# Kernel optimization log

Hardware: AMD Instinct MI355X
Metric: run time of the kernel (lower is better)

## Reference

```python
import jax, jax.numpy as jnp
import numpy as np

NEG_INF = -1e9  # fp32-safe mask value for non-edges
ALPHA = 0.2     # LeakyReLU negative slope


def setup_inputs() -> dict:
    key = jax.random.key(0)
    k1, k2, k3, k4, k5 = jax.random.split(key, 5)
    N, F_in, H, F_out = 4096, 512, 8, 64
    features = jax.random.normal(k1, (N, F_in), dtype=jnp.float32)
    adjacency_matrix = jax.random.randint(k2, (N, N), 0, 2, dtype=jnp.int32)
    W = jax.random.normal(k3, (H, F_in, F_out), dtype=jnp.float32) * (F_in ** -0.5)
    a_src = jax.random.normal(k4, (H, F_out), dtype=jnp.float32) * (F_out ** -0.5)
    a_dst = jax.random.normal(k5, (H, F_out), dtype=jnp.float32) * (F_out ** -0.5)
    return {"features": features, "adjacency_matrix": adjacency_matrix,
            "W": W, "a_src": a_src, "a_dst": a_dst}


def reference(features, adjacency_matrix, W, a_src, a_dst):
    # Per-head linear projection: [H, N, F_out]
    Wh = jnp.einsum('nf,hfo->hno', features, W)
    # Attention logits e_ij = LeakyReLU(a_src . Wh_i + a_dst . Wh_j)
    src = jnp.einsum('hno,ho->hn', Wh, a_src)  # [H, N]
    dst = jnp.einsum('hno,ho->hn', Wh, a_dst)  # [H, N]
    e = jax.nn.leaky_relu(src[:, :, None] + dst[:, None, :], ALPHA)  # [H, N, N]
    mask = (adjacency_matrix > 0)[None, :, :]
    e = jnp.where(mask, e, jnp.asarray(NEG_INF, e.dtype))
    attn = jax.nn.softmax(e, axis=-1)  # adjacency-masked row softmax
    h = jnp.einsum('hij,hjo->hio', attn, Wh)  # [H, N, F_out]
    h = jax.nn.elu(h)
    # concat=True: torch.cat over feature dim -> [N, H*F_out]
    return jnp.transpose(h, (1, 0, 2)).reshape(h.shape[1], -1)
```

## Files before the change

kernel.cpp:

```cpp
#include <hip/hip_runtime.h>
#include <hip/hip_bf16.h>

typedef __bf16 bf16x8 __attribute__((ext_vector_type(8)));
typedef float  f32x4  __attribute__((ext_vector_type(4)));
typedef unsigned short u16x8 __attribute__((ext_vector_type(8)));
typedef unsigned short us4   __attribute__((ext_vector_type(4)));

#define HH    8
#define NN    4096
#define FIN   512
#define FOUT  64
#define ALPHA 0.2f

__global__ __launch_bounds__(256) void k_pack(int* __restrict__ adj) {
    const size_t base = (size_t)blockIdx.x * 8192;
    const int    tid  = threadIdx.x;
    unsigned m = 0;
#pragma unroll
    for (int p = 0; p < 8; ++p) {
        int4 v = *(const int4*)(adj + base + tid * 32 + p * 4);
        m |= (unsigned)(v.x > 0) << (p * 4);
        m |= (unsigned)(v.y > 0) << (p * 4 + 1);
        m |= (unsigned)(v.z > 0) << (p * 4 + 2);
        m |= (unsigned)(v.w > 0) << (p * 4 + 3);
    }
    __syncthreads();
    ((unsigned*)adj)[base + tid] = m;
}

__global__ __launch_bounds__(256) void k_transpose_w(
    const float* __restrict__ Wsrc, __hip_bfloat16* __restrict__ WT) {
    __shared__ __hip_bfloat16 lt[64][65];
    const int h  = blockIdx.x >> 3;
    const int f0 = (blockIdx.x & 7) * 64;
    const int tid = threadIdx.x;
#pragma unroll
    for (int p = 0; p < 16; ++p) {
        int f = p * 4 + (tid >> 6);
        int o = tid & 63;
        lt[f][o] = __float2bfloat16(Wsrc[((size_t)h * FIN + f0 + f) * FOUT + o]);
    }
    __syncthreads();
#pragma unroll
    for (int p = 0; p < 16; ++p) {
        int o = p * 4 + (tid >> 6);
        int f = tid & 63;
        WT[((size_t)h * FOUT + o) * FIN + f0 + f] = lt[f][o];
    }
}

__global__ __launch_bounds__(256) void k_proj(
    const float* __restrict__ feat,
    const __hip_bfloat16* __restrict__ WT,
    const float* __restrict__ a_src,
    const float* __restrict__ a_dst,
    unsigned short* __restrict__ WhT,
    float* __restrict__ srcv,
    unsigned short* __restrict__ Ebf, unsigned short* __restrict__ Fbf) {
    __shared__ alignas(16) __hip_bfloat16 lfeat[32][520];

    const int tid  = threadIdx.x;
    const int tile = blockIdx.x;

#pragma unroll
    for (int p = 0; p < 16; ++p) {
        int idx  = p * 256 + tid;
        int row  = idx >> 7;
        int col4 = (idx & 127) * 4;
        float4 f = *(const float4*)(feat + (size_t)(tile * 32 + row) * FIN + col4);
        __hip_bfloat16* dst = &lfeat[row][col4];
        dst[0] = __float2bfloat16(f.x); dst[1] = __float2bfloat16(f.y);
        dst[2] = __float2bfloat16(f.z); dst[3] = __float2bfloat16(f.w);
    }
    __syncthreads();

    const int h     = blockIdx.y * 4 + (tid >> 6);
    const int lane  = tid & 63;
    const int row16 = lane & 15;
    const int quad  = lane >> 4;

    const unsigned short* WTu = (const unsigned short*)WT + (size_t)h * FOUT * FIN;

    f32x4 acc[2][4] = {};
    for (int k0 = 0; k0 < FIN; k0 += 32) {
        bf16x8 a0 = *(const bf16x8*)&lfeat[row16][k0 + quad * 8];
        bf16x8 a1 = *(const bf16x8*)&lfeat[16 + row16][k0 + quad * 8];
#pragma unroll
        for (int ot = 0; ot < 4; ++ot) {
            bf16x8 b = *(const bf16x8*)(WTu + (size_t)(ot * 16 + row16) * FIN + k0 + quad * 8);
            acc[0][ot] = __builtin_amdgcn_mfma_f32_16x16x32_bf16(a0, b, acc[0][ot], 0, 0, 0);
            acc[1][ot] = __builtin_amdgcn_mfma_f32_16x16x32_bf16(a1, b, acc[1][ot], 0, 0, 0);
        }
    }

#pragma unroll
    for (int g = 0; g < 2; ++g)
#pragma unroll
        for (int ot = 0; ot < 4; ++ot) {
            us4 u;
#pragma unroll
            for (int r = 0; r < 4; ++r)
                u[r] = __builtin_bit_cast(unsigned short, (__bf16)acc[g][ot][r]);
            *(us4*)(WhT + (size_t)(h * FOUT + ot * 16 + row16) * NN
                        + tile * 32 + g * 16 + quad * 4) = u;
        }

    float asv[4], adv[4];
#pragma unroll
    for (int ot = 0; ot < 4; ++ot) {
        asv[ot] = a_src[h * FOUT + ot * 16 + row16];
        adv[ot] = a_dst[h * FOUT + ot * 16 + row16];
    }
#pragma unroll
    for (int g = 0; g < 2; ++g)
#pragma unroll
        for (int r = 0; r < 4; ++r) {
            float ss = 0.f, dd = 0.f;
#pragma unroll
            for (int ot = 0; ot < 4; ++ot) {
                ss += acc[g][ot][r] * asv[ot];
                dd += acc[g][ot][r] * adv[ot];
            }
            ss += __shfl_xor(ss, 1); ss += __shfl_xor(ss, 2);
            ss += __shfl_xor(ss, 4); ss += __shfl_xor(ss, 8);
            dd += __shfl_xor(dd, 1); dd += __shfl_xor(dd, 2);
            dd += __shfl_xor(dd, 4); dd += __shfl_xor(dd, 8);
            if (row16 == 0) {
                int n = tile * 32 + g * 16 + quad * 4 + r;
                srcv[h * NN + n] = ss;
                __bf16 e = (__bf16)__expf(dd);
                __bf16 f = (__bf16)__expf(ALPHA * dd);
                Ebf[h * NN + n] = __builtin_bit_cast(unsigned short, e);
                Fbf[h * NN + n] = __builtin_bit_cast(unsigned short, f);
            }
        }
}

__global__ __launch_bounds__(512, 2) void k_flash(
    const unsigned* __restrict__ maskp,
    const float* __restrict__ srcv,
    const unsigned short* __restrict__ Ebf,
    const unsigned short* __restrict__ Fbf,
    const unsigned short* __restrict__ WhT,
    float* __restrict__ out) {
    __shared__ float lds_stash[2][2][4096];
    __shared__ float lds_l[2][2][64];

    unsigned* lmask = (unsigned*)&lds_stash[0][0][0];

    const int tid   = threadIdx.x;
    const int wv    = tid >> 6;
    const int lane  = tid & 63;
    const int row16 = lane & 15;
    const int quad  = lane >> 4;
    const int h2    = wv & 1;
    const int seg   = wv >> 1;

    const int bx   = blockIdx.x;
    const int hg   = (bx >> 3) & 3;
    const int tile = ((bx >> 5) << 3) | (bx & 7);

#pragma unroll
    for (int p = 0; p < 4; ++p) {
        int tt = tid + p * 512;
        int c  = tt >> 6;
        int o  = (tt & 63) * 16;
        int4 v = *(const int4*)((const char*)maskp
                                + (size_t)(tile * 32 + c) * 32768 + o);
        int row = c * 2 + (o >> 9);
        int dw  = (o & 511) >> 2;
        *(int4*)&lmask[row * 132 + dw] = v;
    }
    __syncthreads();

    const int h   = hg * 2 + h2;
    const int shl = quad * 8;

    float Es[4], Fs[4];
    const unsigned* lm[4];
#pragma unroll
    for (int g = 0; g < 4; ++g) {
        float si = srcv[h * NN + tile * 64 + g * 16 + row16];
        Es[g] = __expf(si);
        Fs[g] = __expf(ALPHA * si);
        lm[g] = &lmask[(g * 16 + row16) * 132 + seg * 32];
    }

    const unsigned short* Eb = Ebf + h * NN + seg * 1024;
    const unsigned short* Fb = Fbf + h * NN + seg * 1024;
    const unsigned short* wh = WhT + (size_t)h * FOUT * NN + seg * 1024;

    bf16x8 ones;
#pragma unroll
    for (int k = 0; k < 8; ++k) ones[k] = (__bf16)1.0f;

    f32x4 acc[4][4] = {};
    f32x4 accl[4]   = {};

#pragma unroll 1
    for (int t = 0; t < 32; ++t) {
        int jj = t * 32 + shl;
        u16x8 ev = *(const u16x8*)(Eb + jj);
        u16x8 fv = *(const u16x8*)(Fb + jj);
        unsigned mb[4];
#pragma unroll
        for (int g = 0; g < 4; ++g) mb[g] = (lm[g][t] >> shl) & 0xffu;

        bf16x8 af[4];
#pragma unroll
        for (int k = 0; k < 8; ++k) {
            float ef = __uint_as_float((unsigned)ev[k] << 16);
            float ff = __uint_as_float((unsigned)fv[k] << 16);
#pragma unroll
            for (int g = 0; g < 4; ++g) {
                float p = fmaxf(ef * Es[g], ff * Fs[g]);
                af[g][k] = (__bf16)(((mb[g] >> k) & 1u) ? p : 0.f);
            }
        }
        bf16x8 b[4];
#pragma unroll
        for (int ot = 0; ot < 4; ++ot)
            b[ot] = *(const bf16x8*)(wh + (size_t)(ot * 16 + row16) * NN + jj);
#pragma unroll
        for (int g = 0; g < 4; ++g) {
#pragma unroll
            for (int ot = 0; ot < 4; ++ot)
                acc[g][ot] = __builtin_amdgcn_mfma_f32_16x16x32_bf16(af[g], b[ot], acc[g][ot], 0, 0, 0);
            accl[g] = __builtin_amdgcn_mfma_f32_16x16x32_bf16(af[g], ones, accl[g], 0, 0, 0);
        }
    }

    __syncthreads();

    if (seg == 1 || seg == 3) {
        float* st = &lds_stash[seg >> 1][h2][0];
#pragma unroll
        for (int g = 0; g < 4; ++g)
#pragma unroll
            for (int ot = 0; ot < 4; ++ot)
#pragma unroll
                for (int r = 0; r < 4; ++r)
                    st[(g * 16 + quad * 4 + r) * 64 + ot * 16 + row16] = acc[g][ot][r];
        if (row16 == 0)
#pragma unroll
            for (int g = 0; g < 4; ++g)
#pragma unroll
                for (int r = 0; r < 4; ++r)
                    lds_l[seg >> 1][h2][g * 16 + quad * 4 + r] = accl[g][r];
    }
    __syncthreads();
    if (seg == 0 || seg == 2) {
        const float* st = &lds_stash[seg >> 1][h2][0];
#pragma unroll
        for (int g = 0; g < 4; ++g) {
#pragma unroll
            for (int ot = 0; ot < 4; ++ot)
#pragma unroll
                for (int r = 0; r < 4; ++r)
                    acc[g][ot][r] += st[(g * 16 + quad * 4 + r) * 64 + ot * 16 + row16];
#pragma unroll
            for (int r = 0; r < 4; ++r)
                accl[g][r] += lds_l[seg >> 1][h2][g * 16 + quad * 4 + r];
        }
    }
    __syncthreads();
    if (seg == 2) {
        float* st = &lds_stash[0][h2][0];
#pragma unroll
        for (int g = 0; g < 4; ++g)
#pragma unroll
            for (int ot = 0; ot < 4; ++ot)
#pragma unroll
                for (int r = 0; r < 4; ++r)
                    st[(g * 16 + quad * 4 + r) * 64 + ot * 16 + row16] = acc[g][ot][r];
        if (row16 == 0)
#pragma unroll
            for (int g = 0; g < 4; ++g)
#pragma unroll
                for (int r = 0; r < 4; ++r)
                    lds_l[0][h2][g * 16 + quad * 4 + r] = accl[g][r];
    }
    __syncthreads();
    if (seg == 0) {
        const float* st = &lds_stash[0][h2][0];
#pragma unroll
        for (int g = 0; g < 4; ++g)
#pragma unroll
            for (int r = 0; r < 4; ++r) {
                int   gqr = g * 16 + quad * 4 + r;
                float l   = accl[g][r] + lds_l[0][h2][gqr];
                float rl  = 1.0f / l;
#pragma unroll
                for (int ot = 0; ot < 4; ++ot) {
                    int   c = ot * 16 + row16;
                    float v = (acc[g][ot][r] + st[gqr * 64 + c]) * rl;
                    float y = v > 0.f ? v : __expf(v) - 1.f;
                    out[(size_t)(tile * 64 + gqr) * (HH * FOUT) + h * FOUT + c] = y;
                }
            }
    }
}

extern "C" void kernel_launch(void* const* d_in, const int* in_sizes, int n_in,
                              void* d_out, int out_size, void* d_ws, size_t ws_size,
                              hipStream_t stream) {
    const float* features = (const float*)d_in[0];
    int*         adj      = (int*)d_in[1];
    const float* W        = (const float*)d_in[2];
    const float* a_src    = (const float*)d_in[3];
    const float* a_dst    = (const float*)d_in[4];
    float*       out      = (float*)d_out;

    char* ws = (char*)d_ws;
    __hip_bfloat16* WT   = (__hip_bfloat16*)(ws);
    unsigned short* WhT  = (unsigned short*)(ws + (512 << 10));
    float*          srcv = (float*)(ws + (512 << 10) + (4 << 20));
    unsigned short* Ebf  = (unsigned short*)(ws + (512 << 10) + (4 << 20) + (128 << 10));
    unsigned short* Fbf  = (unsigned short*)(ws + (512 << 10) + (4 << 20) + (192 << 10));

    k_pack<<<dim3((NN * NN) / 8192), 256, 0, stream>>>(adj);
    k_transpose_w<<<dim3(64), 256, 0, stream>>>(W, WT);
    k_proj<<<dim3(NN / 32, 2), 256, 0, stream>>>(features, WT, a_src, a_dst,
                                                 WhT, srcv, Ebf, Fbf);
    k_flash<<<dim3(256), 512, 0, stream>>>((const unsigned*)adj, srcv, Ebf, Fbf,
                                           WhT, out);
}
```

Measured before the change: 176.0 us.

## Fuse mask packing into projection launch and retile flash kernel per head

```diff
diff --git a/kernel.cpp b/kernel.cpp
--- a/kernel.cpp
+++ b/kernel.cpp
@@ -11,22 +11,6 @@
 #define FIN   512
 #define FOUT  64
 #define ALPHA 0.2f
-
-__global__ __launch_bounds__(256) void k_pack(int* __restrict__ adj) {
-    const size_t base = (size_t)blockIdx.x * 8192;
-    const int    tid  = threadIdx.x;
-    unsigned m = 0;
-#pragma unroll
-    for (int p = 0; p < 8; ++p) {
-        int4 v = *(const int4*)(adj + base + tid * 32 + p * 4);
-        m |= (unsigned)(v.x > 0) << (p * 4);
-        m |= (unsigned)(v.y > 0) << (p * 4 + 1);
-        m |= (unsigned)(v.z > 0) << (p * 4 + 2);
-        m |= (unsigned)(v.w > 0) << (p * 4 + 3);
-    }
-    __syncthreads();
-    ((unsigned*)adj)[base + tid] = m;
-}
 
 __global__ __launch_bounds__(256) void k_transpose_w(
     const float* __restrict__ Wsrc, __hip_bfloat16* __restrict__ WT) {
@@ -49,7 +33,8 @@
     }
 }
 
-__global__ __launch_bounds__(256) void k_proj(
+__global__ __launch_bounds__(256) void k_prep(
+    int* __restrict__ adj,
     const float* __restrict__ feat,
     const __hip_bfloat16* __restrict__ WT,
     const float* __restrict__ a_src,
@@ -59,8 +44,27 @@
     unsigned short* __restrict__ Ebf, unsigned short* __restrict__ Fbf) {
     __shared__ alignas(16) __hip_bfloat16 lfeat[32][520];
 
-    const int tid  = threadIdx.x;
-    const int tile = blockIdx.x;
+    const int tid = threadIdx.x;
+
+    if (blockIdx.x < 2048) {
+        const size_t base = (size_t)blockIdx.x * 8192;
+        unsigned m = 0;
+#pragma unroll
+        for (int p = 0; p < 8; ++p) {
+            int4 v = *(const int4*)(adj + base + tid * 32 + p * 4);
+            m |= (unsigned)(v.x > 0) << (p * 4);
+            m |= (unsigned)(v.y > 0) << (p * 4 + 1);
+            m |= (unsigned)(v.z > 0) << (p * 4 + 2);
+            m |= (unsigned)(v.w > 0) << (p * 4 + 3);
+        }
+        __syncthreads();
+        ((unsigned*)adj)[base + tid] = m;
+        return;
+    }
+
+    const int pb   = blockIdx.x - 2048;
+    const int tile = pb & 127;
+    const int hgy  = pb >> 7;
 
 #pragma unroll
     for (int p = 0; p < 16; ++p) {
@@ -74,7 +78,7 @@
     }
     __syncthreads();
 
-    const int h     = blockIdx.y * 4 + (tid >> 6);
+    const int h     = hgy * 4 + (tid >> 6);
     const int lane  = tid & 63;
     const int row16 = lane & 15;
     const int quad  = lane >> 4;
@@ -143,161 +147,168 @@
     const unsigned short* __restrict__ Fbf,
     const unsigned short* __restrict__ WhT,
     float* __restrict__ out) {
-    __shared__ float lds_stash[2][2][4096];
-    __shared__ float lds_l[2][2][64];
-
-    unsigned* lmask = (unsigned*)&lds_stash[0][0][0];
+    __shared__ float st[2][128 * 68];
+    __shared__ float lds_l[2][128];
+
+    unsigned* lmask = (unsigned*)&st[0][0];
 
     const int tid   = threadIdx.x;
-    const int wv    = tid >> 6;
+    const int seg   = tid >> 6;
     const int lane  = tid & 63;
     const int row16 = lane & 15;
     const int quad  = lane >> 4;
-    const int h2    = wv & 1;
-    const int seg   = wv >> 1;
-
-    const int bx   = blockIdx.x;
-    const int hg   = (bx >> 3) & 3;
-    const int tile = ((bx >> 5) << 3) | (bx & 7);
-
-#pragma unroll
-    for (int p = 0; p < 4; ++p) {
+    const int shl   = quad * 8;
+    const int tile  = blockIdx.x;
+    const int h     = blockIdx.y;
+
+#pragma unroll
+    for (int p = 0; p < 8; ++p) {
         int tt = tid + p * 512;
         int c  = tt >> 6;
         int o  = (tt & 63) * 16;
         int4 v = *(const int4*)((const char*)maskp
-                                + (size_t)(tile * 32 + c) * 32768 + o);
+                                + (size_t)(tile * 64 + c) * 32768 + o);
         int row = c * 2 + (o >> 9);
         int dw  = (o & 511) >> 2;
         *(int4*)&lmask[row * 132 + dw] = v;
     }
     __syncthreads();
 
-    const int h   = hg * 2 + h2;
-    const int shl = quad * 8;
-
-    float Es[4], Fs[4];
-    const unsigned* lm[4];
-#pragma unroll
-    for (int g = 0; g < 4; ++g) {
-        float si = srcv[h * NN + tile * 64 + g * 16 + row16];
+    float Es[8], Fs[8];
+#pragma unroll
+    for (int g = 0; g < 8; ++g) {
+        float si = srcv[h * NN + tile * 128 + g * 16 + row16];
         Es[g] = __expf(si);
         Fs[g] = __expf(ALPHA * si);
-        lm[g] = &lmask[(g * 16 + row16) * 132 + seg * 32];
-    }
-
-    const unsigned short* Eb = Ebf + h * NN + seg * 1024;
-    const unsigned short* Fb = Fbf + h * NN + seg * 1024;
-    const unsigned short* wh = WhT + (size_t)h * FOUT * NN + seg * 1024;
+    }
+    const int mbase = row16 * 132 + seg * 16;
+
+    const unsigned short* Eb = Ebf + h * NN + seg * 512;
+    const unsigned short* Fb = Fbf + h * NN + seg * 512;
+    const unsigned short* wh = WhT + (size_t)h * FOUT * NN + seg * 512;
 
     bf16x8 ones;
 #pragma unroll
     for (int k = 0; k < 8; ++k) ones[k] = (__bf16)1.0f;
 
-    f32x4 acc[4][4] = {};
-    f32x4 accl[4]   = {};
+    f32x4 acc[8][4] = {};
+    f32x4 accl[8]   = {};
 
 #pragma unroll 1
-    for (int t = 0; t < 32; ++t) {
+    for (int t = 0; t < 16; ++t) {
         int jj = t * 32 + shl;
         u16x8 ev = *(const u16x8*)(Eb + jj);
         u16x8 fv = *(const u16x8*)(Fb + jj);
-        unsigned mb[4];
-#pragma unroll
-        for (int g = 0; g < 4; ++g) mb[g] = (lm[g][t] >> shl) & 0xffu;
-
-        bf16x8 af[4];
-#pragma unroll
-        for (int k = 0; k < 8; ++k) {
-            float ef = __uint_as_float((unsigned)ev[k] << 16);
-            float ff = __uint_as_float((unsigned)fv[k] << 16);
-#pragma unroll
-            for (int g = 0; g < 4; ++g) {
-                float p = fmaxf(ef * Es[g], ff * Fs[g]);
-                af[g][k] = (__bf16)(((mb[g] >> k) & 1u) ? p : 0.f);
-            }
-        }
         bf16x8 b[4];
 #pragma unroll
         for (int ot = 0; ot < 4; ++ot)
             b[ot] = *(const bf16x8*)(wh + (size_t)(ot * 16 + row16) * NN + jj);
-#pragma unroll
-        for (int g = 0; g < 4; ++g) {
+
+        float ef[8], ff[8];
+#pragma unroll
+        for (int k = 0; k < 8; ++k) {
+            ef[k] = __uint_as_float((unsigned)ev[k] << 16);
+            ff[k] = __uint_as_float((unsigned)fv[k] << 16);
+        }
+
+#pragma unroll
+        for (int gp = 0; gp < 4; ++gp) {
+            const int g0 = gp * 2, g1 = g0 + 1;
+            unsigned mb0 = (lmask[mbase + g0 * 2112 + t] >> shl) & 0xffu;
+            unsigned mb1 = (lmask[mbase + g1 * 2112 + t] >> shl) & 0xffu;
+            bf16x8 af0, af1;
+#pragma unroll
+            for (int k = 0; k < 8; ++k) {
+                float p0 = fmaxf(ef[k] * Es[g0], ff[k] * Fs[g0]);
+                float p1 = fmaxf(ef[k] * Es[g1], ff[k] * Fs[g1]);
+                af0[k] = (__bf16)(((mb0 >> k) & 1u) ? p0 : 0.f);
+                af1[k] = (__bf16)(((mb1 >> k) & 1u) ? p1 : 0.f);
+            }
+#pragma unroll
+            for (int ot = 0; ot < 4; ++ot) {
+                acc[g0][ot] = __builtin_amdgcn_mfma_f32_16x16x32_bf16(af0, b[ot], acc[g0][ot], 0, 0, 0);
+                acc[g1][ot] = __builtin_amdgcn_mfma_f32_16x16x32_bf16(af1, b[ot], acc[g1][ot], 0, 0, 0);
+            }
+            accl[g0] = __builtin_amdgcn_mfma_f32_16x16x32_bf16(af0, ones, accl[g0], 0, 0, 0);
+            accl[g1] = __builtin_amdgcn_mfma_f32_16x16x32_bf16(af1, ones, accl[g1], 0, 0, 0);
+        }
+    }
+
+    __syncthreads();
+
+    auto stash = [&](int buf) {
+#pragma unroll
+        for (int g = 0; g < 8; ++g)
 #pragma unroll
             for (int ot = 0; ot < 4; ++ot)
-                acc[g][ot] = __builtin_amdgcn_mfma_f32_16x16x32_bf16(af[g], b[ot], acc[g][ot], 0, 0, 0);
-            accl[g] = __builtin_amdgcn_mfma_f32_16x16x32_bf16(af[g], ones, accl[g], 0, 0, 0);
-        }
-    }
-
-    __syncthreads();
-
-    if (seg == 1 || seg == 3) {
-        float* st = &lds_stash[seg >> 1][h2][0];
-#pragma unroll
-        for (int g = 0; g < 4; ++g)
+#pragma unroll
+                for (int r = 0; r < 4; ++r)
+                    st[buf][(g * 16 + quad * 4 + r) * 68 + ot * 16 + row16] = acc[g][ot][r];
+        if (row16 == 0)
+#pragma unroll
+            for (int g = 0; g < 8; ++g)
+#pragma unroll
+                for (int r = 0; r < 4; ++r)
+                    lds_l[buf][g * 16 + quad * 4 + r] = accl[g][r];
+    };
+    auto addin = [&](int buf) {
+#pragma unroll
+        for (int g = 0; g < 8; ++g) {
 #pragma unroll
             for (int ot = 0; ot < 4; ++ot)
 #pragma unroll
                 for (int r = 0; r < 4; ++r)
-                    st[(g * 16 + quad * 4 + r) * 64 + ot * 16 + row16] = acc[g][ot][r];
-        if (row16 == 0)
-#pragma unroll
-            for (int g = 0; g < 4; ++g)
-#pragma unroll
-                for (int r = 0; r < 4; ++r)
-                    lds_l[seg >> 1][h2][g * 16 + quad * 4 + r] = accl[g][r];
-    }
-    __syncthreads();
-    if (seg == 0 || seg == 2) {
-        const float* st = &lds_stash[seg >> 1][h2][0];
-#pragma unroll
-        for (int g = 0; g < 4; ++g) {
-#pragma unroll
-            for (int ot = 0; ot < 4; ++ot)
-#pragma unroll
-                for (int r = 0; r < 4; ++r)
-                    acc[g][ot][r] += st[(g * 16 + quad * 4 + r) * 64 + ot * 16 + row16];
+                    acc[g][ot][r] += st[buf][(g * 16 + quad * 4 + r) * 68 + ot * 16 + row16];
 #pragma unroll
             for (int r = 0; r < 4; ++r)
-                accl[g][r] += lds_l[seg >> 1][h2][g * 16 + quad * 4 + r];
-        }
-    }
-    __syncthreads();
-    if (seg == 2) {
-        float* st = &lds_stash[0][h2][0];
-#pragma unroll
-        for (int g = 0; g < 4; ++g)
-#pragma unroll
-            for (int ot = 0; ot < 4; ++ot)
-#pragma unroll
-                for (int r = 0; r < 4; ++r)
-                    st[(g * 16 + quad * 4 + r) * 64 + ot * 16 + row16] = acc[g][ot][r];
-        if (row16 == 0)
-#pragma unroll
-            for (int g = 0; g < 4; ++g)
-#pragma unroll
-                for (int r = 0; r < 4; ++r)
-                    lds_l[0][h2][g * 16 + quad * 4 + r] = accl[g][r];
-    }
+                accl[g][r] += lds_l[buf][g * 16 + quad * 4 + r];
+        }
+    };
+
+    if (seg == 1) stash(0);
+    if (seg == 3) stash(1);
+    __syncthreads();
+    if (seg == 0) addin(0);
+    if (seg == 2) addin(1);
+    __syncthreads();
+    if (seg == 5) stash(0);
+    if (seg == 7) stash(1);
+    __syncthreads();
+    if (seg == 4) addin(0);
+    if (seg == 6) addin(1);
+    __syncthreads();
+    if (seg == 2) stash(0);
+    if (seg == 6) stash(1);
+    __syncthreads();
+    if (seg == 0) addin(0);
+    if (seg == 4) addin(1);
+    __syncthreads();
+    if (seg == 4) stash(0);
     __syncthreads();
     if (seg == 0) {
-        const float* st = &lds_stash[0][h2][0];
-#pragma unroll
-        for (int g = 0; g < 4; ++g)
+        addin(0);
+#pragma unroll
+        for (int g = 0; g < 8; ++g)
 #pragma unroll
             for (int r = 0; r < 4; ++r) {
                 int   gqr = g * 16 + quad * 4 + r;
-                float l   = accl[g][r] + lds_l[0][h2][gqr];
-                float rl  = 1.0f / l;
+                float rl  = 1.0f / accl[g][r];
 #pragma unroll
                 for (int ot = 0; ot < 4; ++ot) {
-                    int   c = ot * 16 + row16;
-                    float v = (acc[g][ot][r] + st[gqr * 64 + c]) * rl;
+                    float v = acc[g][ot][r] * rl;
                     float y = v > 0.f ? v : __expf(v) - 1.f;
-                    out[(size_t)(tile * 64 + gqr) * (HH * FOUT) + h * FOUT + c] = y;
+                    st[0][gqr * 68 + ot * 16 + row16] = y;
                 }
             }
+    }
+    __syncthreads();
+#pragma unroll
+    for (int p = 0; p < 4; ++p) {
+        int f    = tid + p * 512;
+        int row  = f >> 4;
+        int col4 = (f & 15) * 4;
+        float4 v = *(const float4*)&st[0][row * 68 + col4];
+        *(float4*)&out[(size_t)(tile * 128 + row) * (HH * FOUT) + h * FOUT + col4] = v;
     }
 }
 
@@ -318,10 +329,9 @@
     unsigned short* Ebf  = (unsigned short*)(ws + (512 << 10) + (4 << 20) + (128 << 10));
     unsigned short* Fbf  = (unsigned short*)(ws + (512 << 10) + (4 << 20) + (192 << 10));
 
-    k_pack<<<dim3((NN * NN) / 8192), 256, 0, stream>>>(adj);
     k_transpose_w<<<dim3(64), 256, 0, stream>>>(W, WT);
-    k_proj<<<dim3(NN / 32, 2), 256, 0, stream>>>(features, WT, a_src, a_dst,
+    k_prep<<<dim3(2048 + 256), 256, 0, stream>>>(adj, features, WT, a_src, a_dst,
                                                  WhT, srcv, Ebf, Fbf);
-    k_flash<<<dim3(256), 512, 0, stream>>>((const unsigned*)adj, srcv, Ebf, Fbf,
-                                           WhT, out);
+    k_flash<<<dim3(32, 8), 512, 0, stream>>>((const unsigned*)adj, srcv, Ebf, Fbf,
+                                             WhT, out);
 }
```

After: 174.7 us. No clear change (-0.8%).
